# Performance work log

Measured on AMD Instinct MI355X. Metric: run time of the kernel, lower is better.

## Reference

```python
import jax, jax.numpy as jnp
import numpy as np

N_AA = 20
A = 15
D_FEAT = 128
CA_IDX = 1
NUM_FUNCS = 3
FREQ_BANDS = jnp.array([1.0, 2.0, 3.0, 1.0, 0.5, 1.0 / 3.0], dtype=jnp.float32)


def setup_inputs() -> dict:
    key = jax.random.key(0)
    ks = jax.random.split(key, 16)
    b, L = 16, 1024
    d_in = D_FEAT + N_AA * A * 3 + 3 * (NUM_FUNCS * 2 * 2 + 1) + D_FEAT  # 1195
    inp = {
        "seq": jax.random.randint(ks[0], (b, L), 0, N_AA),
        "xyz": jax.random.normal(ks[1], (b, L, A, 3), dtype=jnp.float32),
        "dihedrals": jax.random.normal(ks[2], (b, L, 3), dtype=jnp.float32),
        "chain_idx": jax.random.randint(ks[3], (b, L), 0, 10),
        "orientation": jax.random.normal(ks[4], (b, L, 3, 3), dtype=jnp.float32),
        "atom_mask": jnp.ones((b, L, A), dtype=bool),
        "aa_emb": jax.random.normal(ks[5], (N_AA, D_FEAT), dtype=jnp.float32),
        "chain_emb": jax.random.normal(ks[6], (10, D_FEAT), dtype=jnp.float32).at[0].set(0.0),  # padding_idx=0
        "W1": jax.random.normal(ks[7], (d_in, 2 * D_FEAT), dtype=jnp.float32) * 0.02,
        "b1": jnp.zeros((2 * D_FEAT,), dtype=jnp.float32),
        "W2": jax.random.normal(ks[8], (2 * D_FEAT, D_FEAT), dtype=jnp.float32) * 0.02,
        "b2": jnp.zeros((D_FEAT,), dtype=jnp.float32),
        "W3": jax.random.normal(ks[9], (D_FEAT, D_FEAT), dtype=jnp.float32) * 0.02,
        "b3": jnp.zeros((D_FEAT,), dtype=jnp.float32),
        "W4": jax.random.normal(ks[10], (D_FEAT, D_FEAT), dtype=jnp.float32) * 0.02,
        "b4": jnp.zeros((D_FEAT,), dtype=jnp.float32),
    }
    return inp


def angular_encoding(x):
    # x: (..., d_in) -> (..., d_in * 13)
    xe = x[..., None]  # (..., d_in, 1)
    enc = jnp.concatenate([xe, jnp.sin(FREQ_BANDS * xe), jnp.cos(FREQ_BANDS * xe)], axis=-1)
    return enc.reshape(*x.shape[:-1], -1)


def reference(seq, xyz, dihedrals, chain_idx, orientation, atom_mask,
              aa_emb, chain_emb, W1, b1, W2, b2, W3, b3, W4, b4):
    b, L = seq.shape
    aa_type_feat = aa_emb[seq]  # (b, L, d_feat)

    # local coordinates relative to CA, rotated into local frame via O^T
    xyz_rel = xyz - xyz[:, :, CA_IDX:CA_IDX + 1, :]  # (b, L, A, 3)
    xyz_local = jnp.einsum('blji,blaj->blai', orientation, xyz_rel)  # O^T @ xyz_rel

    # one-hot select: place xyz_local in the slot of the residue's aa type
    onehot = jax.nn.one_hot(seq, N_AA, dtype=xyz.dtype)  # (b, L, 20)
    coord_feat = (onehot[:, :, :, None, None] * xyz_local[:, :, None, :, :]).reshape(b, L, N_AA * A * 3)

    dihedral_feat = angular_encoding(dihedrals)  # (b, L, 39)

    chain_feat = chain_emb[chain_idx] * (chain_idx != 0)[..., None].astype(xyz.dtype)  # padding_idx=0

    x = jnp.concatenate([aa_type_feat, coord_feat, dihedral_feat, chain_feat], axis=-1)
    h = jax.nn.relu(x @ W1 + b1)
    h = jax.nn.relu(h @ W2 + b2)
    h = jax.nn.relu(h @ W3 + b3)
    return h @ W4 + b4
```

## Files before the change

### kernel.cpp

```cpp
#include <hip/hip_runtime.h>
#include <math.h>

#define N_AA    20
#define NATOM   15
#define TM      16
#define MAXBL   16384
#define MAXBLK  (MAXBL / TM + N_AA)
#define NWAVE   16

#define FSX  104
#define HSX  264
#define H2SX 136

typedef __attribute__((ext_vector_type(8))) short bf16x8;
typedef __attribute__((ext_vector_type(4))) float f32x4;

#define W1F_SLOTS  (N_AA * 16 * 3 * 64)
#define W2F_SLOTS  (8 * 8 * 64)
#define W34F_SLOTS (8 * 4 * 64)
#define TOT_SLOTS  (W1F_SLOTS + W2F_SLOTS + 2 * W34F_SLOTS)

__device__ __forceinline__ unsigned short f2bf(float x) {
    unsigned u = __float_as_uint(x);
    return (unsigned short)((u + 0x7FFFu + ((u >> 16) & 1u)) >> 16);
}
__device__ __forceinline__ float bf2f(unsigned short h) {
    return __uint_as_float(((unsigned)h) << 16);
}
__device__ __forceinline__ void put2(unsigned short* H, unsigned short* L, int idx, float v) {
    unsigned short hi = f2bf(v);
    H[idx] = hi;
    L[idx] = f2bf(v - bf2f(hi));
}

__global__ __launch_bounds__(1024) void prep_kernel(
    const int* __restrict__ seq, const float* __restrict__ aa_emb,
    const float* __restrict__ chain_emb, const float* __restrict__ W1,
    const float* __restrict__ W2, const float* __restrict__ W3, const float* __restrict__ W4,
    int BL,
    float* __restrict__ aaT, float* __restrict__ chT,
    int* __restrict__ bucket_start, int* __restrict__ blk_type,
    int* __restrict__ blk_chunk, int* __restrict__ rowidx,
    unsigned short* __restrict__ W1fH, unsigned short* __restrict__ W1fL,
    unsigned short* __restrict__ W2fH, unsigned short* __restrict__ W2fL,
    unsigned short* __restrict__ W3fH, unsigned short* __restrict__ W3fL,
    unsigned short* __restrict__ W4fH, unsigned short* __restrict__ W4fL)
{
    const int t = threadIdx.x;
    const int b = blockIdx.x;

    if (b < 30) {
        if (t < 256) {
            if (b < N_AA) {
                const float* e = aa_emb + b * 128;
                float acc = 0.f;
                #pragma unroll 8
                for (int k = 0; k < 128; ++k)
                    acc += e[k] * W1[(size_t)k * 256 + t];
                aaT[b * 256 + t] = acc;
            } else {
                const int c = b - N_AA;
                const float* e = chain_emb + c * 128;
                float acc = 0.f;
                #pragma unroll 8
                for (int k = 0; k < 128; ++k)
                    acc += e[k] * W1[(size_t)(1067 + k) * 256 + t];
                chT[c * 256 + t] = acc;
            }
        }
        return;
    }

    if (b >= 31) {
        const int slot = (b - 31) * 1024 + t;
        if (slot >= TOT_SLOTS) return;
        float v[8];
        unsigned short *dH, *dL;
        if (slot < W1F_SLOTS) {
            const int g = slot / 3072, r1 = slot % 3072;
            const int tile = r1 / 192, chunk = (r1 / 64) % 3, lane = r1 % 64;
            const int n  = tile * 16 + (lane & 15);
            const int kb = chunk * 32 + (lane >> 4) * 8;
            #pragma unroll
            for (int j = 0; j < 8; ++j) {
                const int k = kb + j;
                float x = 0.f;
                if (k < 45)       x = W1[(size_t)(128 + g * 45 + k) * 256 + n];
                else if (k < 84)  x = W1[(size_t)(1028 + k - 45) * 256 + n];
                v[j] = x;
            }
            dH = W1fH + (size_t)slot * 8; dL = W1fL + (size_t)slot * 8;
        } else if (slot < W1F_SLOTS + W2F_SLOTS) {
            const int s = slot - W1F_SLOTS;
            const int tile = s / 512, chunk = (s / 64) % 8, lane = s % 64;
            const int n  = tile * 16 + (lane & 15);
            const int kb = chunk * 32 + (lane >> 4) * 8;
            #pragma unroll
            for (int j = 0; j < 8; ++j) v[j] = W2[(size_t)(kb + j) * 128 + n];
            dH = W2fH + (size_t)s * 8; dL = W2fL + (size_t)s * 8;
        } else if (slot < W1F_SLOTS + W2F_SLOTS + W34F_SLOTS) {
            const int s = slot - W1F_SLOTS - W2F_SLOTS;
            const int tile = s / 256, chunk = (s / 64) % 4, lane = s % 64;
            const int n  = tile * 16 + (lane & 15);
            const int kb = chunk * 32 + (lane >> 4) * 8;
            #pragma unroll
            for (int j = 0; j < 8; ++j) v[j] = W3[(size_t)(kb + j) * 128 + n];
            dH = W3fH + (size_t)s * 8; dL = W3fL + (size_t)s * 8;
        } else {
            const int s = slot - W1F_SLOTS - W2F_SLOTS - W34F_SLOTS;
            const int tile = s / 256, chunk = (s / 64) % 4, lane = s % 64;
            const int n  = tile * 16 + (lane & 15);
            const int kb = chunk * 32 + (lane >> 4) * 8;
            #pragma unroll
            for (int j = 0; j < 8; ++j) v[j] = W4[(size_t)(kb + j) * 128 + n];
            dH = W4fH + (size_t)s * 8; dL = W4fL + (size_t)s * 8;
        }
        #pragma unroll
        for (int j = 0; j < 8; ++j) {
            const unsigned short hi = f2bf(v[j]);
            dH[j] = hi;
            dL[j] = f2bf(v[j] - bf2f(hi));
        }
        return;
    }

    __shared__ int sseq[MAXBL];
    __shared__ int hist[NWAVE][N_AA];
    __shared__ int wcur[NWAVE][N_AA];
    __shared__ int bs[N_AA + 1];
    __shared__ int blkoff[N_AA + 1];

    const int w = t >> 6;
    for (int i = t; i < BL; i += 1024) sseq[i] = seq[i];
    if (t < NWAVE * N_AA) hist[t / N_AA][t % N_AA] = 0;
    __syncthreads();
    for (int i = t; i < BL; i += 1024) atomicAdd(&hist[w][sseq[i]], 1);
    __syncthreads();
    if (t == 0) {
        int runr = 0, runb = 0;
        for (int g = 0; g < N_AA; ++g) {
            int s = 0;
            #pragma unroll
            for (int ww = 0; ww < NWAVE; ++ww) s += hist[ww][g];
            bs[g] = runr; runr += s;
            blkoff[g] = runb; runb += (s + TM - 1) / TM;
        }
        bs[N_AA] = runr; blkoff[N_AA] = runb;
    }
    __syncthreads();
    if (t <= N_AA) bucket_start[t] = bs[t];
    if (t < NWAVE * N_AA) {
        const int w2 = t / N_AA, g2 = t % N_AA;
        int o = bs[g2];
        for (int ww = 0; ww < w2; ++ww) o += hist[ww][g2];
        wcur[w2][g2] = o;
    }
    const int nblk = blkoff[N_AA];
    for (int i = t; i < MAXBLK; i += 1024) {
        if (i < nblk) {
            int g = 0;
            while (blkoff[g + 1] <= i) ++g;
            blk_type[i]  = g;
            blk_chunk[i] = i - blkoff[g];
        } else blk_type[i] = -1;
    }
    __syncthreads();
    for (int i = t; i < BL; i += 1024) {
        const int pos = atomicAdd(&wcur[w][sseq[i]], 1);
        rowidx[pos] = i;
    }
}

__global__ __launch_bounds__(256, 4) void fused_kernel(
    const int* __restrict__ chain_idx, const float* __restrict__ xyz,
    const float* __restrict__ dihedrals, const float* __restrict__ orientation,
    const float* __restrict__ b1, const float* __restrict__ b2,
    const float* __restrict__ b3, const float* __restrict__ b4,
    const float* __restrict__ aaT, const float* __restrict__ chT,
    const int* __restrict__ bucket_start, const int* __restrict__ blk_type,
    const int* __restrict__ blk_chunk, const int* __restrict__ rowidx,
    const unsigned short* __restrict__ W1fH, const unsigned short* __restrict__ W1fL,
    const unsigned short* __restrict__ W2fH, const unsigned short* __restrict__ W2fL,
    const unsigned short* __restrict__ W3fH, const unsigned short* __restrict__ W3fL,
    const unsigned short* __restrict__ W4fH, const unsigned short* __restrict__ W4fL,
    float* __restrict__ out)
{
    __shared__ __align__(16) unsigned short featH[TM * FSX], featL[TM * FSX];
    __shared__ __align__(16) unsigned short hAH[TM * HSX],  hAL[TM * HSX];
    __shared__ __align__(16) unsigned short hBH[TM * H2SX], hBL[TM * H2SX];
    __shared__ int s_row[TM], s_rowld[TM], s_chain[TM];

    const int t = threadIdx.x;
    const int g = blk_type[blockIdx.x];
    if (g < 0) return;
    const int chunk  = blk_chunk[blockIdx.x];
    const int bstart = bucket_start[g] + chunk * TM;
    const int nrows  = min(TM, bucket_start[g + 1] - bstart);

    if (t < TM) {
        const bool valid = (t < nrows);
        const int rl = rowidx[valid ? (bstart + t) : bstart];
        s_row[t]   = valid ? rl : -1;
        s_rowld[t] = rl;
        s_chain[t] = chain_idx[rl];
    }
    __syncthreads();

    if (t < TM * NATOM) {
        const int r = t / NATOM, a = t % NATOM;
        const int rl = s_rowld[r];
        const float* xr = xyz + (size_t)rl * (NATOM * 3);
        const float cax = xr[3], cay = xr[4], caz = xr[5];
        const float rx = xr[a*3+0] - cax;
        const float ry = xr[a*3+1] - cay;
        const float rz = xr[a*3+2] - caz;
        const float* O = orientation + (size_t)rl * 9;
        put2(featH, featL, r * FSX + a*3 + 0, O[0]*rx + O[3]*ry + O[6]*rz);
        put2(featH, featL, r * FSX + a*3 + 1, O[1]*rx + O[4]*ry + O[7]*rz);
        put2(featH, featL, r * FSX + a*3 + 2, O[2]*rx + O[5]*ry + O[8]*rz);
    }
    if (t < TM * 3) {
        const int r = t / 3, d = t % 3;
        const float x = dihedrals[(size_t)s_rowld[r] * 3 + d];
        const int base = r * FSX + 45 + d * 13;
        const float F3 = (float)(1.0 / 3.0);
        put2(featH, featL, base + 0, x);
        put2(featH, featL, base + 1, sinf(x));      put2(featH, featL, base + 2, sinf(2.f*x));
        put2(featH, featL, base + 3, sinf(3.f*x));  put2(featH, featL, base + 4, sinf(x));
        put2(featH, featL, base + 5, sinf(0.5f*x)); put2(featH, featL, base + 6, sinf(F3*x));
        put2(featH, featL, base + 7, cosf(x));      put2(featH, featL, base + 8, cosf(2.f*x));
        put2(featH, featL, base + 9, cosf(3.f*x));  put2(featH, featL, base +10, cosf(x));
        put2(featH, featL, base +11, cosf(0.5f*x)); put2(featH, featL, base +12, cosf(F3*x));
    }
    if (t < TM) {
        #pragma unroll
        for (int k = 84; k < 96; ++k) { featH[t * FSX + k] = 0; featL[t * FSX + k] = 0; }
    }
    __syncthreads();

    const int wave = t >> 6, lane = t & 63, quad = lane >> 4, nid = lane & 15;
    const f32x4 zero = {0.f, 0.f, 0.f, 0.f};

    {
        f32x4 acc[4] = {zero, zero, zero, zero};
        for (int c = 0; c < 3; ++c) {
            const bf16x8 aH = *(const bf16x8*)(featH + nid * FSX + c * 32 + quad * 8);
            const bf16x8 aL = *(const bf16x8*)(featL + nid * FSX + c * 32 + quad * 8);
            #pragma unroll
            for (int tt = 0; tt < 4; ++tt) {
                const size_t off = ((size_t)((g * 16 + (wave * 4 + tt)) * 3 + c) * 64 + lane) * 8;
                const bf16x8 bH = *(const bf16x8*)(W1fH + off);
                const bf16x8 bL = *(const bf16x8*)(W1fL + off);
                acc[tt] = __builtin_amdgcn_mfma_f32_16x16x32_bf16(aH, bH, acc[tt], 0, 0, 0);
                acc[tt] = __builtin_amdgcn_mfma_f32_16x16x32_bf16(aH, bL, acc[tt], 0, 0, 0);
                acc[tt] = __builtin_amdgcn_mfma_f32_16x16x32_bf16(aL, bH, acc[tt], 0, 0, 0);
            }
        }
        #pragma unroll
        for (int tt = 0; tt < 4; ++tt) {
            const int j = (wave * 4 + tt) * 16 + nid;
            const float cb = b1[j] + aaT[g * 256 + j];
            #pragma unroll
            for (int r = 0; r < 4; ++r) {
                const int row = quad * 4 + r;
                float v = acc[tt][r] + cb + chT[s_chain[row] * 256 + j];
                v = fmaxf(v, 0.f);
                put2(hAH, hAL, row * HSX + j, v);
            }
        }
    }
    __syncthreads();

    {
        f32x4 acc[2] = {zero, zero};
        for (int c = 0; c < 8; ++c) {
            const bf16x8 aH = *(const bf16x8*)(hAH + nid * HSX + c * 32 + quad * 8);
            const bf16x8 aL = *(const bf16x8*)(hAL + nid * HSX + c * 32 + quad * 8);
            #pragma unroll
            for (int tt = 0; tt < 2; ++tt) {
                const size_t off = ((size_t)((wave * 2 + tt) * 8 + c) * 64 + lane) * 8;
                const bf16x8 bH = *(const bf16x8*)(W2fH + off);
                const bf16x8 bL = *(const bf16x8*)(W2fL + off);
                acc[tt] = __builtin_amdgcn_mfma_f32_16x16x32_bf16(aH, bH, acc[tt], 0, 0, 0);
                acc[tt] = __builtin_amdgcn_mfma_f32_16x16x32_bf16(aH, bL, acc[tt], 0, 0, 0);
                acc[tt] = __builtin_amdgcn_mfma_f32_16x16x32_bf16(aL, bH, acc[tt], 0, 0, 0);
            }
        }
        #pragma unroll
        for (int tt = 0; tt < 2; ++tt) {
            const int j = (wave * 2 + tt) * 16 + nid;
            const float bb = b2[j];
            #pragma unroll
            for (int r = 0; r < 4; ++r) {
                const int row = quad * 4 + r;
                float v = fmaxf(acc[tt][r] + bb, 0.f);
                put2(hBH, hBL, row * H2SX + j, v);
            }
        }
    }
    __syncthreads();

    {
        f32x4 acc[2] = {zero, zero};
        for (int c = 0; c < 4; ++c) {
            const bf16x8 aH = *(const bf16x8*)(hBH + nid * H2SX + c * 32 + quad * 8);
            const bf16x8 aL = *(const bf16x8*)(hBL + nid * H2SX + c * 32 + quad * 8);
            #pragma unroll
            for (int tt = 0; tt < 2; ++tt) {
                const size_t off = ((size_t)((wave * 2 + tt) * 4 + c) * 64 + lane) * 8;
                const bf16x8 bH = *(const bf16x8*)(W3fH + off);
                const bf16x8 bL = *(const bf16x8*)(W3fL + off);
                acc[tt] = __builtin_amdgcn_mfma_f32_16x16x32_bf16(aH, bH, acc[tt], 0, 0, 0);
                acc[tt] = __builtin_amdgcn_mfma_f32_16x16x32_bf16(aH, bL, acc[tt], 0, 0, 0);
                acc[tt] = __builtin_amdgcn_mfma_f32_16x16x32_bf16(aL, bH, acc[tt], 0, 0, 0);
            }
        }
        #pragma unroll
        for (int tt = 0; tt < 2; ++tt) {
            const int j = (wave * 2 + tt) * 16 + nid;
            const float bb = b3[j];
            #pragma unroll
            for (int r = 0; r < 4; ++r) {
                const int row = quad * 4 + r;
                float v = fmaxf(acc[tt][r] + bb, 0.f);
                put2(hAH, hAL, row * HSX + j, v);
            }
        }
    }
    __syncthreads();

    {
        f32x4 acc[2] = {zero, zero};
        for (int c = 0; c < 4; ++c) {
            const bf16x8 aH = *(const bf16x8*)(hAH + nid * HSX + c * 32 + quad * 8);
            const bf16x8 aL = *(const bf16x8*)(hAL + nid * HSX + c * 32 + quad * 8);
            #pragma unroll
            for (int tt = 0; tt < 2; ++tt) {
                const size_t off = ((size_t)((wave * 2 + tt) * 4 + c) * 64 + lane) * 8;
                const bf16x8 bH = *(const bf16x8*)(W4fH + off);
                const bf16x8 bL = *(const bf16x8*)(W4fL + off);
                acc[tt] = __builtin_amdgcn_mfma_f32_16x16x32_bf16(aH, bH, acc[tt], 0, 0, 0);
                acc[tt] = __builtin_amdgcn_mfma_f32_16x16x32_bf16(aH, bL, acc[tt], 0, 0, 0);
                acc[tt] = __builtin_amdgcn_mfma_f32_16x16x32_bf16(aL, bH, acc[tt], 0, 0, 0);
            }
        }
        #pragma unroll
        for (int tt = 0; tt < 2; ++tt) {
            const int j = (wave * 2 + tt) * 16 + nid;
            const float bb = b4[j];
            #pragma unroll
            for (int r = 0; r < 4; ++r) {
                const int row = quad * 4 + r;
                const int orow = s_row[row];
                if (orow >= 0) out[(size_t)orow * 128 + j] = acc[tt][r] + bb;
            }
        }
    }
}

extern "C" void kernel_launch(void* const* d_in, const int* in_sizes, int n_in,
                              void* d_out, int out_size, void* d_ws, size_t ws_size,
                              hipStream_t stream) {
    const int*   seq    = (const int*)d_in[0];
    const float* xyz    = (const float*)d_in[1];
    const float* dihed  = (const float*)d_in[2];
    const int*   chain  = (const int*)d_in[3];
    const float* orient = (const float*)d_in[4];
    const float* aa_emb = (const float*)d_in[6];
    const float* ch_emb = (const float*)d_in[7];
    const float* W1 = (const float*)d_in[8];
    const float* b1 = (const float*)d_in[9];
    const float* W2 = (const float*)d_in[10];
    const float* b2 = (const float*)d_in[11];
    const float* W3 = (const float*)d_in[12];
    const float* b3 = (const float*)d_in[13];
    const float* W4 = (const float*)d_in[14];
    const float* b4 = (const float*)d_in[15];
    float* out = (float*)d_out;

    const int BL = in_sizes[0];

    char* p = (char*)d_ws;
    float* aaT = (float*)p;            p += 20 * 256 * 4;
    float* chT = (float*)p;            p += 10 * 256 * 4;
    int* bucket_start = (int*)p;       p += 32 * 4;
    int* blk_type     = (int*)p;       p += MAXBLK * 4;
    int* blk_chunk    = (int*)p;       p += MAXBLK * 4;
    int* rowidx       = (int*)p;       p += MAXBL * 4;
    p += ((16 - ((uintptr_t)p & 15)) & 15);
    unsigned short* W1fH = (unsigned short*)p; p += (size_t)W1F_SLOTS * 8 * 2;
    unsigned short* W1fL = (unsigned short*)p; p += (size_t)W1F_SLOTS * 8 * 2;
    unsigned short* W2fH = (unsigned short*)p; p += (size_t)W2F_SLOTS * 8 * 2;
    unsigned short* W2fL = (unsigned short*)p; p += (size_t)W2F_SLOTS * 8 * 2;
    unsigned short* W3fH = (unsigned short*)p; p += (size_t)W34F_SLOTS * 8 * 2;
    unsigned short* W3fL = (unsigned short*)p; p += (size_t)W34F_SLOTS * 8 * 2;
    unsigned short* W4fH = (unsigned short*)p; p += (size_t)W34F_SLOTS * 8 * 2;
    unsigned short* W4fL = (unsigned short*)p;

    const int nprep  = 31 + (TOT_SLOTS + 1023) / 1024;
    const int nfused = BL / TM + N_AA;

    prep_kernel<<<nprep, 1024, 0, stream>>>(seq, aa_emb, ch_emb, W1, W2, W3, W4, BL,
                                            aaT, chT, bucket_start, blk_type, blk_chunk, rowidx,
                                            W1fH, W1fL, W2fH, W2fL, W3fH, W3fL, W4fH, W4fL);
    fused_kernel<<<nfused, 256, 0, stream>>>(chain, xyz, dihed, orient,
                                             b1, b2, b3, b4, aaT, chT,
                                             bucket_start, blk_type, blk_chunk, rowidx,
                                             W1fH, W1fL, W2fH, W2fL, W3fH, W3fL, W4fH, W4fL,
                                             out);
}
```

Before: 132.4 us.

## Alias feature and layer-2 LDS buffers, raise occupancy, and pack prep blocks

The feature staging buffer and the layer-2 activation buffer now share one LDS region, with an extra barrier before the layer-2 outputs overwrite it. This cuts shared memory per block so the launch bound can ask for five blocks per CU instead of four. The prep kernel packs four embedding-projection tables per 1024-thread block instead of using 256 of 1024 threads, which shrinks its grid. Duplicate sin/cos calls are also reused. The added barrier and a tighter register budget could offset some of the occupancy gain.

```diff
diff --git a/kernel.cpp b/kernel.cpp
--- a/kernel.cpp
+++ b/kernel.cpp
@@ -49,30 +49,32 @@
     const int t = threadIdx.x;
     const int b = blockIdx.x;
 
-    if (b < 30) {
-        if (t < 256) {
-            if (b < N_AA) {
-                const float* e = aa_emb + b * 128;
+    if (b < 8) {
+        const int tab = b * 4 + (t >> 8);
+        const int col = t & 255;
+        if (tab < 30) {
+            if (tab < N_AA) {
+                const float* e = aa_emb + tab * 128;
                 float acc = 0.f;
                 #pragma unroll 8
                 for (int k = 0; k < 128; ++k)
-                    acc += e[k] * W1[(size_t)k * 256 + t];
-                aaT[b * 256 + t] = acc;
+                    acc += e[k] * W1[(size_t)k * 256 + col];
+                aaT[tab * 256 + col] = acc;
             } else {
-                const int c = b - N_AA;
+                const int c = tab - N_AA;
                 const float* e = chain_emb + c * 128;
                 float acc = 0.f;
                 #pragma unroll 8
                 for (int k = 0; k < 128; ++k)
-                    acc += e[k] * W1[(size_t)(1067 + k) * 256 + t];
-                chT[c * 256 + t] = acc;
+                    acc += e[k] * W1[(size_t)(1067 + k) * 256 + col];
+                chT[c * 256 + col] = acc;
             }
         }
         return;
     }
 
-    if (b >= 31) {
-        const int slot = (b - 31) * 1024 + t;
+    if (b >= 9) {
+        const int slot = (b - 9) * 1024 + t;
         if (slot >= TOT_SLOTS) return;
         float v[8];
         unsigned short *dH, *dL;
@@ -171,7 +173,7 @@
     }
 }
 
-__global__ __launch_bounds__(256, 4) void fused_kernel(
+__global__ __launch_bounds__(256, 5) void fused_kernel(
     const int* __restrict__ chain_idx, const float* __restrict__ xyz,
     const float* __restrict__ dihedrals, const float* __restrict__ orientation,
     const float* __restrict__ b1, const float* __restrict__ b2,
@@ -185,10 +187,16 @@
     const unsigned short* __restrict__ W4fH, const unsigned short* __restrict__ W4fL,
     float* __restrict__ out)
 {
-    __shared__ __align__(16) unsigned short featH[TM * FSX], featL[TM * FSX];
-    __shared__ __align__(16) unsigned short hAH[TM * HSX],  hAL[TM * HSX];
-    __shared__ __align__(16) unsigned short hBH[TM * H2SX], hBL[TM * H2SX];
+    __shared__ __align__(16) unsigned short smemA[2 * TM * HSX];
+    __shared__ __align__(16) unsigned short smemB[2 * TM * H2SX];
     __shared__ int s_row[TM], s_rowld[TM], s_chain[TM];
+
+    unsigned short* hAH   = smemA;
+    unsigned short* hAL   = smemA + TM * HSX;
+    unsigned short* featH = smemB;
+    unsigned short* featL = smemB + TM * FSX;
+    unsigned short* hBH   = smemB;
+    unsigned short* hBL   = smemB + TM * H2SX;
 
     const int t = threadIdx.x;
     const int g = blk_type[blockIdx.x];
@@ -224,12 +232,13 @@
         const float x = dihedrals[(size_t)s_rowld[r] * 3 + d];
         const int base = r * FSX + 45 + d * 13;
         const float F3 = (float)(1.0 / 3.0);
+        const float s1 = sinf(x), c1 = cosf(x);
         put2(featH, featL, base + 0, x);
-        put2(featH, featL, base + 1, sinf(x));      put2(featH, featL, base + 2, sinf(2.f*x));
-        put2(featH, featL, base + 3, sinf(3.f*x));  put2(featH, featL, base + 4, sinf(x));
+        put2(featH, featL, base + 1, s1);           put2(featH, featL, base + 2, sinf(2.f*x));
+        put2(featH, featL, base + 3, sinf(3.f*x));  put2(featH, featL, base + 4, s1);
         put2(featH, featL, base + 5, sinf(0.5f*x)); put2(featH, featL, base + 6, sinf(F3*x));
-        put2(featH, featL, base + 7, cosf(x));      put2(featH, featL, base + 8, cosf(2.f*x));
-        put2(featH, featL, base + 9, cosf(3.f*x));  put2(featH, featL, base +10, cosf(x));
+        put2(featH, featL, base + 7, c1);           put2(featH, featL, base + 8, cosf(2.f*x));
+        put2(featH, featL, base + 9, cosf(3.f*x));  put2(featH, featL, base +10, c1);
         put2(featH, featL, base +11, cosf(0.5f*x)); put2(featH, featL, base +12, cosf(F3*x));
     }
     if (t < TM) {
@@ -286,6 +295,7 @@
                 acc[tt] = __builtin_amdgcn_mfma_f32_16x16x32_bf16(aL, bH, acc[tt], 0, 0, 0);
             }
         }
+        __syncthreads();
         #pragma unroll
         for (int tt = 0; tt < 2; ++tt) {
             const int j = (wave * 2 + tt) * 16 + nid;
@@ -397,7 +407,7 @@
     unsigned short* W4fH = (unsigned short*)p; p += (size_t)W34F_SLOTS * 8 * 2;
     unsigned short* W4fL = (unsigned short*)p;
 
-    const int nprep  = 31 + (TOT_SLOTS + 1023) / 1024;
+    const int nprep  = 9 + (TOT_SLOTS + 1023) / 1024;
     const int nfused = BL / TM + N_AA;
 
     prep_kernel<<<nprep, 1024, 0, stream>>>(seq, aa_emb, ch_emb, W1, W2, W3, W4, BL,
```

Result: faster. 121.9 us (-7.9%).
